# Performance work log

Hardware: AMD Instinct MI355X
Metric: run time of the kernel (lower is better)

The kernel has to match this reference:

```python
import jax, jax.numpy as jnp
import numpy as np

N_NODES = 100000
N_EDGES = 1600000
N_GRAPHS = 1000
NODES_PER_GRAPH = N_NODES // N_GRAPHS
IN_DIM, HID_DIM, OUT_DIM = 32, 64, 32


def setup_inputs() -> dict:
    key = jax.random.key(0)
    k_x, k_src, k_dst, k_w1, k_w2 = jax.random.split(key, 5)
    x = jax.random.normal(k_x, (N_NODES, IN_DIM), dtype=jnp.float32)
    src = jax.random.randint(k_src, (N_EDGES,), 0, N_NODES, dtype=jnp.int32)
    dst = jax.random.randint(k_dst, (N_EDGES,), 0, N_NODES, dtype=jnp.int32)
    edge_index = jnp.stack([src, dst], axis=0)
    batch = (jnp.arange(N_NODES, dtype=jnp.int32) // NODES_PER_GRAPH)
    W1 = jax.random.normal(k_w1, (IN_DIM, HID_DIM), dtype=jnp.float32) / np.sqrt(IN_DIM)
    b1 = jnp.zeros((HID_DIM,), dtype=jnp.float32)
    W2 = jax.random.normal(k_w2, (HID_DIM, OUT_DIM), dtype=jnp.float32) / np.sqrt(HID_DIM)
    b2 = jnp.zeros((OUT_DIM,), dtype=jnp.float32)
    return {"x": x, "edge_index": edge_index, "batch": batch,
            "W1": W1, "b1": b1, "W2": W2, "b2": b2}


def _gcn_conv(x, W, b, src, dst, deg_inv_sqrt):
    # PyG GCNConv: out = D^{-1/2}(A+I)D^{-1/2} X W + b, deg includes self-loops
    h = x @ W  # [N, F]
    norm = deg_inv_sqrt[src] * deg_inv_sqrt[dst]  # [E]
    agg = jax.ops.segment_sum(h[src] * norm[:, None], dst, num_segments=N_NODES)
    # self-loop contribution: norm = deg^{-1/2} * deg^{-1/2} = 1/deg
    agg = agg + h * (deg_inv_sqrt * deg_inv_sqrt)[:, None]
    return agg + b


def reference(x, edge_index, batch, W1, b1, W2, b2):
    src, dst = edge_index[0], edge_index[1]
    # degree at target nodes, with self-loops
    deg = 1.0 + jax.ops.segment_sum(jnp.ones_like(dst, dtype=x.dtype), dst,
                                    num_segments=N_NODES)
    deg_inv_sqrt = jax.lax.rsqrt(deg)
    h = jax.nn.relu(_gcn_conv(x, W1, b1, src, dst, deg_inv_sqrt))
    h = _gcn_conv(h, W2, b2, src, dst, deg_inv_sqrt)
    # per-graph mean pooling (fused segment mean)
    sums = jax.ops.segment_sum(h, batch, num_segments=N_GRAPHS)
    counts = jax.ops.segment_sum(jnp.ones((h.shape[0],), dtype=h.dtype), batch,
                                 num_segments=N_GRAPHS)
    return sums / counts[:, None]
```

## Files before the change

kernel.cpp:

```cpp
#include <hip/hip_runtime.h>

#define IN_DIM 32
#define HID_DIM 64
#define OUT_DIM 32

#define MAXBUCK 1024
#define CAP 2560
#define EPB 8192

typedef unsigned int u32;
typedef unsigned short u16;
typedef unsigned long long u64;
typedef __attribute__((ext_vector_type(8))) short bf16x8;
typedef __attribute__((ext_vector_type(4))) float f32x4;

static __device__ __forceinline__ u32 bf16rne(float f) {
    u32 u = __float_as_uint(f);
    return (u + 0x7FFFu + ((u >> 16) & 1u)) >> 16;
}
static __device__ __forceinline__ float blo(u32 u) { return __uint_as_float(u << 16); }
static __device__ __forceinline__ float bhi(u32 u) { return __uint_as_float(u & 0xFFFF0000u); }

__global__ __launch_bounds__(1024) void k_bin(const int* __restrict__ src,
                                              const int* __restrict__ dst,
                                              int* __restrict__ cursor,
                                              int* __restrict__ binned,
                                              int E, int nbuck, int npg, u32 M) {
    __shared__ int lcnt[MAXBUCK];
    __shared__ int lbase[MAXBUCK];
    int t = threadIdx.x;
    if (t < MAXBUCK) lcnt[t] = 0;
    __syncthreads();
    int base = blockIdx.x * EPB;
    int dreg[8], breg[8];
#pragma unroll
    for (int k = 0; k < 8; k++) {
        int e = base + k * 1024 + t;
        dreg[k] = (e < E) ? dst[e] : -1;
    }
#pragma unroll
    for (int k = 0; k < 8; k++) {
        if (dreg[k] >= 0) {
            breg[k] = (int)(((u64)(u32)dreg[k] * M) >> 38);
            atomicAdd(&lcnt[breg[k]], 1);
        }
    }
    __syncthreads();
    if (t < nbuck) {
        int c = lcnt[t];
        if (c) lbase[t] = atomicAdd(&cursor[t], c);
        lcnt[t] = 0;
    }
    __syncthreads();
#pragma unroll
    for (int k = 0; k < 8; k++) {
        if (dreg[k] >= 0) {
            int bk = breg[k];
            int dl = dreg[k] - bk * npg;
            int loc = lbase[bk] + atomicAdd(&lcnt[bk], 1);
            if (loc < CAP)
                binned[bk * CAP + loc] = (dl << 17) | src[base + k * 1024 + t];
        }
    }
}

__global__ __launch_bounds__(256) void k_csr(const int* __restrict__ binned,
                                             const int* __restrict__ cursor,
                                             const float* __restrict__ x,
                                             int2* __restrict__ row,
                                             float* __restrict__ dis,
                                             u16* __restrict__ g,
                                             int* __restrict__ meta,
                                             int N, int npg) {
    __shared__ int sEdge[CAP];
    __shared__ int sH[4][128];
    __shared__ int sExcl[128];
    __shared__ int sCur[128];
    __shared__ float sdis[128];
    __shared__ int wsum[2];
    int b = blockIdx.x;
    int t = threadIdx.x;
    int wid = t >> 6;
    int s0 = b * CAP;
    int cnt = cursor[b];
    if (cnt > CAP) cnt = CAP;

    for (int k = t; k < 4 * 128; k += 256) ((int*)sH)[k] = 0;
    __syncthreads();

    for (int k = t; k < cnt; k += 256) {
        int p = binned[s0 + k];
        sEdge[k] = p;
        atomicAdd(&sH[wid][p >> 17], 1);
    }
    __syncthreads();

    if (t < 128) {
        int myv = sH[0][t] + sH[1][t] + sH[2][t] + sH[3][t];
        int lane = t & 63;
        int incl = myv;
#pragma unroll
        for (int o = 1; o < 64; o <<= 1) {
            int up = __shfl_up(incl, o);
            if (lane >= o) incl += up;
        }
        if (lane == 63) wsum[t >> 6] = incl;
        sExcl[t] = incl - myv;
        sCur[t] = 0;
        sH[0][t] = myv;
    }
    __syncthreads();
    if (t < 128) {
        int exclv = sExcl[t] + ((t >= 64) ? wsum[0] : 0);
        sExcl[t] = exclv;
        int myv = sH[0][t];
        float d = rsqrtf(1.0f + (float)myv);
        sdis[t] = d;
        int node = b * npg + t;
        if (t < npg && node < N) {
            row[node] = make_int2(s0 + exclv, s0 + exclv + myv);
            dis[node] = d;
        }
    }
    __syncthreads();

    for (int k = t; k < cnt; k += 256) {
        int p = sEdge[k];
        int dl = p >> 17;
        int pos = sExcl[dl] + atomicAdd(&sCur[dl], 1);
        meta[s0 + pos] = p & 0x1FFFF;
    }

    int nbLo = b * npg;
    int nn = N - nbLo;
    if (nn > npg) nn = npg;
    if (nn < 0) nn = 0;
    int halfE = nn * 16;
    const float* xb = x + (size_t)nbLo * 32;
    u32* gb = (u32*)(g + (size_t)nbLo * 32);
    for (int j = t; j < halfE; j += 256) {
        int e0 = j * 2;
        float dd = sdis[e0 >> 5];
        gb[j] = bf16rne(dd * xb[e0]) | (bf16rne(dd * xb[e0 + 1]) << 16);
    }
}

__global__ __launch_bounds__(256) void k_agg(const u16* __restrict__ g,
                                             const int* __restrict__ meta,
                                             const int2* __restrict__ row,
                                             const float* __restrict__ dis,
                                             u16* __restrict__ outf, int N) {
    int gid = blockIdx.x * 256 + threadIdx.x;
    int i = gid >> 5;
    if (i >= N) return;
    int l = threadIdx.x & 31;
    int grp = (l >> 2) & 7;
    int sub = l & 3;
    const uint4* gv = (const uint4*)g;

    float a0 = 0.f, a1 = 0.f, a2 = 0.f, a3 = 0.f;
    float a4 = 0.f, a5 = 0.f, a6 = 0.f, a7 = 0.f;
    int2 rw = row[i];
    int e = rw.x, end = rw.y;
    for (; e + 16 <= end; e += 16) {
        int s0 = meta[e + grp];
        int s1 = meta[e + 8 + grp];
        uint4 v0 = gv[s0 * 4 + sub];
        uint4 v1 = gv[s1 * 4 + sub];
        a0 += blo(v0.x); a1 += bhi(v0.x); a2 += blo(v0.y); a3 += bhi(v0.y);
        a4 += blo(v0.z); a5 += bhi(v0.z); a6 += blo(v0.w); a7 += bhi(v0.w);
        a0 += blo(v1.x); a1 += bhi(v1.x); a2 += blo(v1.y); a3 += bhi(v1.y);
        a4 += blo(v1.z); a5 += bhi(v1.z); a6 += blo(v1.w); a7 += bhi(v1.w);
    }
    if (e + grp < end) {
        uint4 v = gv[meta[e + grp] * 4 + sub];
        a0 += blo(v.x); a1 += bhi(v.x); a2 += blo(v.y); a3 += bhi(v.y);
        a4 += blo(v.z); a5 += bhi(v.z); a6 += blo(v.w); a7 += bhi(v.w);
    }
    if (e + 8 + grp < end) {
        uint4 v = gv[meta[e + 8 + grp] * 4 + sub];
        a0 += blo(v.x); a1 += bhi(v.x); a2 += blo(v.y); a3 += bhi(v.y);
        a4 += blo(v.z); a5 += bhi(v.z); a6 += blo(v.w); a7 += bhi(v.w);
    }
#pragma unroll
    for (int m = 4; m <= 16; m <<= 1) {
        a0 += __shfl_xor(a0, m); a1 += __shfl_xor(a1, m);
        a2 += __shfl_xor(a2, m); a3 += __shfl_xor(a3, m);
        a4 += __shfl_xor(a4, m); a5 += __shfl_xor(a5, m);
        a6 += __shfl_xor(a6, m); a7 += __shfl_xor(a7, m);
    }
    if (grp == 0) {
        uint4 sv = gv[i * 4 + sub];
        float d = dis[i];
        u32 o0 = bf16rne(d * (a0 + blo(sv.x))) | (bf16rne(d * (a1 + bhi(sv.x))) << 16);
        u32 o1 = bf16rne(d * (a2 + blo(sv.y))) | (bf16rne(d * (a3 + bhi(sv.y))) << 16);
        u32 o2 = bf16rne(d * (a4 + blo(sv.z))) | (bf16rne(d * (a5 + bhi(sv.z))) << 16);
        u32 o3 = bf16rne(d * (a6 + blo(sv.w))) | (bf16rne(d * (a7 + bhi(sv.w))) << 16);
        ((uint4*)outf)[i * 4 + sub] = make_uint4(o0, o1, o2, o3);
    }
}

__global__ __launch_bounds__(256) void k_mlp(const u16* __restrict__ aggX,
                                             const float* __restrict__ W1,
                                             const float* __restrict__ b1,
                                             const float* __restrict__ W2,
                                             const float* __restrict__ dis,
                                             u16* __restrict__ t2, int N) {
    __shared__ float sHls[4][16 * 65];
    int t = threadIdx.x;
    int w = t >> 6;
    int L = t & 63;
    int q = L >> 4;
    int col = L & 15;
    int base = blockIdx.x * 64 + w * 16;

    int arow = base + col;
    uint4 av = (arow < N) ? ((const uint4*)aggX)[(size_t)arow * 4 + q]
                          : make_uint4(0, 0, 0, 0);
    bf16x8 afrag = *(bf16x8*)&av;

    bf16x8 b1f[4];
#pragma unroll
    for (int nt = 0; nt < 4; nt++) {
#pragma unroll
        for (int jj = 0; jj < 8; jj++)
            b1f[nt][jj] = (short)bf16rne(W1[(q * 8 + jj) * HID_DIM + nt * 16 + col]);
    }
    bf16x8 b2f[2][2];
#pragma unroll
    for (int ks = 0; ks < 2; ks++)
#pragma unroll
        for (int nt = 0; nt < 2; nt++) {
#pragma unroll
            for (int jj = 0; jj < 8; jj++)
                b2f[ks][nt][jj] =
                    (short)bf16rne(W2[(ks * 32 + q * 8 + jj) * OUT_DIM + nt * 16 + col]);
        }

#pragma unroll
    for (int nt = 0; nt < 4; nt++) {
        float bias = b1[nt * 16 + col];
        f32x4 c = {bias, bias, bias, bias};
        c = __builtin_amdgcn_mfma_f32_16x16x32_bf16(afrag, b1f[nt], c, 0, 0, 0);
#pragma unroll
        for (int r = 0; r < 4; r++)
            sHls[w][(q * 4 + r) * 65 + nt * 16 + col] = fmaxf(c[r], 0.0f);
    }
    __syncthreads();

    bf16x8 a2[2];
#pragma unroll
    for (int ks = 0; ks < 2; ks++) {
#pragma unroll
        for (int jj = 0; jj < 8; jj++)
            a2[ks][jj] = (short)bf16rne(sHls[w][col * 65 + ks * 32 + q * 8 + jj]);
    }

    f32x4 C2[2];
#pragma unroll
    for (int nt = 0; nt < 2; nt++) {
        f32x4 c = {0.f, 0.f, 0.f, 0.f};
        c = __builtin_amdgcn_mfma_f32_16x16x32_bf16(a2[0], b2f[0][nt], c, 0, 0, 0);
        c = __builtin_amdgcn_mfma_f32_16x16x32_bf16(a2[1], b2f[1][nt], c, 0, 0, 0);
        C2[nt] = c;
    }

#pragma unroll
    for (int r = 0; r < 4; r++) {
        int node = base + q * 4 + r;
        if (node < N) {
            float dd = dis[node];
            t2[(size_t)node * 32 + col]      = (u16)bf16rne(dd * C2[0][r]);
            t2[(size_t)node * 32 + 16 + col] = (u16)bf16rne(dd * C2[1][r]);
        }
    }
}

__global__ __launch_bounds__(256) void k_pool2(const int* __restrict__ binned,
                                               const int* __restrict__ cursor,
                                               const u16* __restrict__ gB,
                                               const float* __restrict__ dis,
                                               const float* __restrict__ b2,
                                               float* __restrict__ out,
                                               int N, int npg, float inv_npg) {
    __shared__ float sdis[128];
    __shared__ float sacc[32];
    int b = blockIdx.x;
    int t = threadIdx.x;
    if (t < 128) {
        int node = b * npg + t;
        sdis[t] = (t < npg && node < N) ? dis[node] : 0.0f;
    }
    if (t < 32) sacc[t] = 0.0f;
    __syncthreads();

    int s0 = b * CAP;
    int cnt = cursor[b];
    if (cnt > CAP) cnt = CAP;
    int sub = t & 3;
    int et = t >> 2;
    const uint4* gv = (const uint4*)gB;

    float a0 = 0.f, a1 = 0.f, a2 = 0.f, a3 = 0.f;
    float a4 = 0.f, a5 = 0.f, a6 = 0.f, a7 = 0.f;
    int e = et;
    int p0 = 0;
    uint4 v0 = make_uint4(0, 0, 0, 0);
    bool have = (e < cnt);
    if (have) { p0 = binned[s0 + e]; v0 = gv[(p0 & 0x1FFFF) * 4 + sub]; }
    for (; e + 64 < cnt; e += 64) {
        int p1 = binned[s0 + e + 64];
        uint4 v1 = gv[(p1 & 0x1FFFF) * 4 + sub];
        float w = sdis[p0 >> 17];
        a0 = fmaf(w, blo(v0.x), a0); a1 = fmaf(w, bhi(v0.x), a1);
        a2 = fmaf(w, blo(v0.y), a2); a3 = fmaf(w, bhi(v0.y), a3);
        a4 = fmaf(w, blo(v0.z), a4); a5 = fmaf(w, bhi(v0.z), a5);
        a6 = fmaf(w, blo(v0.w), a6); a7 = fmaf(w, bhi(v0.w), a7);
        p0 = p1; v0 = v1;
    }
    if (have) {
        float w = sdis[p0 >> 17];
        a0 = fmaf(w, blo(v0.x), a0); a1 = fmaf(w, bhi(v0.x), a1);
        a2 = fmaf(w, blo(v0.y), a2); a3 = fmaf(w, bhi(v0.y), a3);
        a4 = fmaf(w, blo(v0.z), a4); a5 = fmaf(w, bhi(v0.z), a5);
        a6 = fmaf(w, blo(v0.w), a6); a7 = fmaf(w, bhi(v0.w), a7);
    }
#pragma unroll
    for (int m = 4; m <= 32; m <<= 1) {
        a0 += __shfl_xor(a0, m); a1 += __shfl_xor(a1, m);
        a2 += __shfl_xor(a2, m); a3 += __shfl_xor(a3, m);
        a4 += __shfl_xor(a4, m); a5 += __shfl_xor(a5, m);
        a6 += __shfl_xor(a6, m); a7 += __shfl_xor(a7, m);
    }
    if ((t & 63) < 4) {
        atomicAdd(&sacc[sub * 8 + 0], a0);
        atomicAdd(&sacc[sub * 8 + 1], a1);
        atomicAdd(&sacc[sub * 8 + 2], a2);
        atomicAdd(&sacc[sub * 8 + 3], a3);
        atomicAdd(&sacc[sub * 8 + 4], a4);
        atomicAdd(&sacc[sub * 8 + 5], a5);
        atomicAdd(&sacc[sub * 8 + 6], a6);
        atomicAdd(&sacc[sub * 8 + 7], a7);
    }

    float accs = 0.0f;
    int elems = npg * 32;
    const u16* gbase = gB + (size_t)b * npg * 32;
    int nbLo = b * npg;
    for (int k = t; k < elems; k += 256) {
        int node = k >> 5;
        if (nbLo + node < N)
            accs = fmaf(sdis[node], __uint_as_float((u32)gbase[k] << 16), accs);
    }
    atomicAdd(&sacc[t & 31], accs);
    __syncthreads();

    if (t < 32)
        out[b * 32 + t] = fmaf(sacc[t], inv_npg, b2[t]);
}

extern "C" void kernel_launch(void* const* d_in, const int* in_sizes, int n_in,
                              void* d_out, int out_size, void* d_ws, size_t ws_size,
                              hipStream_t stream) {
    const float* x   = (const float*)d_in[0];
    const int* eidx  = (const int*)d_in[1];
    const float* W1  = (const float*)d_in[3];
    const float* b1  = (const float*)d_in[4];
    const float* W2  = (const float*)d_in[5];
    const float* b2  = (const float*)d_in[6];
    float* out       = (float*)d_out;

    const int N = in_sizes[0] / IN_DIM;
    const int E = in_sizes[1] / 2;
    const int G = out_size / OUT_DIM;
    const int npg = N / G;
    const int nbuck = G;
    const int* src = eidx;
    const int* dst = eidx + E;
    const u32 M = (u32)(((1ull << 38) + npg - 1) / (u64)npg);

    char* ws = (char*)d_ws;
    size_t off = 0;
    auto alloc = [&](size_t bytes) -> char* {
        char* p = ws + off;
        off = (off + bytes + 255) & ~(size_t)255;
        return p;
    };
    int*   cursor = (int*)alloc(MAXBUCK * sizeof(int));
    int2*  row    = (int2*)alloc((size_t)N * sizeof(int2));
    float* dis    = (float*)alloc((size_t)N * sizeof(float));
    int*   binned = (int*)alloc((size_t)nbuck * CAP * sizeof(int));
    int*   meta   = (int*)alloc((size_t)nbuck * CAP * sizeof(int));
    u16*   g      = (u16*)alloc((size_t)N * IN_DIM * sizeof(u16));
    u16*   bufA   = (u16*)alloc((size_t)N * IN_DIM * sizeof(u16));
    u16*   bufB   = (u16*)alloc((size_t)N * OUT_DIM * sizeof(u16));
    (void)ws_size;

    hipMemsetAsync(cursor, 0, MAXBUCK * sizeof(int), stream);

    k_bin<<<(E + EPB - 1) / EPB, 1024, 0, stream>>>(src, dst, cursor, binned,
                                                    E, nbuck, npg, M);
    k_csr<<<nbuck, 256, 0, stream>>>(binned, cursor, x, row, dis, g, meta, N, npg);
    k_agg<<<((size_t)N * 32 + 255) / 256, 256, 0, stream>>>(g, meta, row, dis, bufA, N);
    k_mlp<<<(N + 63) / 64, 256, 0, stream>>>(bufA, W1, b1, W2, dis, bufB, N);
    k_pool2<<<nbuck, 256, 0, stream>>>(binned, cursor, bufB, dis, b2, out,
                                       N, npg, 1.0f / (float)npg);
}
```

Measured before the change: 161.7 us.

## Drop CSR build; fuse layer-1 aggregation and MLP per graph bucket via LDS atomics

The CSR construction (prefix scan and meta scatter) goes away. Layer-1 aggregation is now done per destination bucket with shared-memory float atomics straight from the binned edge list, and it is fused with the two-layer MFMA MLP in one kernel per graph, which removes the bufA round trip and one launch. The self-loop pooling term is computed inside the fused kernel and passed to the pool kernel, which now runs 512 threads with a simpler unrolled gather loop. In exchange, LDS atomic contention rises and the order of float summation changes.

After: 392.3 us. +142.6%, slower.

```diff
diff --git a/kernel.cpp b/kernel.cpp
--- a/kernel.cpp
+++ b/kernel.cpp
@@ -64,20 +64,14 @@
     }
 }
 
-__global__ __launch_bounds__(256) void k_csr(const int* __restrict__ binned,
+__global__ __launch_bounds__(256) void k_deg(const int* __restrict__ binned,
                                              const int* __restrict__ cursor,
                                              const float* __restrict__ x,
-                                             int2* __restrict__ row,
                                              float* __restrict__ dis,
                                              u16* __restrict__ g,
-                                             int* __restrict__ meta,
                                              int N, int npg) {
-    __shared__ int sEdge[CAP];
     __shared__ int sH[4][128];
-    __shared__ int sExcl[128];
-    __shared__ int sCur[128];
     __shared__ float sdis[128];
-    __shared__ int wsum[2];
     int b = blockIdx.x;
     int t = threadIdx.x;
     int wid = t >> 6;
@@ -87,49 +81,17 @@
 
     for (int k = t; k < 4 * 128; k += 256) ((int*)sH)[k] = 0;
     __syncthreads();
-
-    for (int k = t; k < cnt; k += 256) {
-        int p = binned[s0 + k];
-        sEdge[k] = p;
-        atomicAdd(&sH[wid][p >> 17], 1);
-    }
-    __syncthreads();
-
+    for (int k = t; k < cnt; k += 256)
+        atomicAdd(&sH[wid][binned[s0 + k] >> 17], 1);
+    __syncthreads();
     if (t < 128) {
-        int myv = sH[0][t] + sH[1][t] + sH[2][t] + sH[3][t];
-        int lane = t & 63;
-        int incl = myv;
-#pragma unroll
-        for (int o = 1; o < 64; o <<= 1) {
-            int up = __shfl_up(incl, o);
-            if (lane >= o) incl += up;
-        }
-        if (lane == 63) wsum[t >> 6] = incl;
-        sExcl[t] = incl - myv;
-        sCur[t] = 0;
-        sH[0][t] = myv;
-    }
-    __syncthreads();
-    if (t < 128) {
-        int exclv = sExcl[t] + ((t >= 64) ? wsum[0] : 0);
-        sExcl[t] = exclv;
-        int myv = sH[0][t];
-        float d = rsqrtf(1.0f + (float)myv);
+        int deg = sH[0][t] + sH[1][t] + sH[2][t] + sH[3][t];
+        float d = rsqrtf(1.0f + (float)deg);
         sdis[t] = d;
         int node = b * npg + t;
-        if (t < npg && node < N) {
-            row[node] = make_int2(s0 + exclv, s0 + exclv + myv);
-            dis[node] = d;
-        }
-    }
-    __syncthreads();
-
-    for (int k = t; k < cnt; k += 256) {
-        int p = sEdge[k];
-        int dl = p >> 17;
-        int pos = sExcl[dl] + atomicAdd(&sCur[dl], 1);
-        meta[s0 + pos] = p & 0x1FFFF;
-    }
+        if (t < npg && node < N) dis[node] = d;
+    }
+    __syncthreads();
 
     int nbLo = b * npg;
     int nn = N - nbLo;
@@ -145,79 +107,68 @@
     }
 }
 
-__global__ __launch_bounds__(256) void k_agg(const u16* __restrict__ g,
-                                             const int* __restrict__ meta,
-                                             const int2* __restrict__ row,
-                                             const float* __restrict__ dis,
-                                             u16* __restrict__ outf, int N) {
-    int gid = blockIdx.x * 256 + threadIdx.x;
-    int i = gid >> 5;
-    if (i >= N) return;
-    int l = threadIdx.x & 31;
-    int grp = (l >> 2) & 7;
-    int sub = l & 3;
-    const uint4* gv = (const uint4*)g;
-
-    float a0 = 0.f, a1 = 0.f, a2 = 0.f, a3 = 0.f;
-    float a4 = 0.f, a5 = 0.f, a6 = 0.f, a7 = 0.f;
-    int2 rw = row[i];
-    int e = rw.x, end = rw.y;
-    for (; e + 16 <= end; e += 16) {
-        int s0 = meta[e + grp];
-        int s1 = meta[e + 8 + grp];
-        uint4 v0 = gv[s0 * 4 + sub];
-        uint4 v1 = gv[s1 * 4 + sub];
-        a0 += blo(v0.x); a1 += bhi(v0.x); a2 += blo(v0.y); a3 += bhi(v0.y);
-        a4 += blo(v0.z); a5 += bhi(v0.z); a6 += blo(v0.w); a7 += bhi(v0.w);
-        a0 += blo(v1.x); a1 += bhi(v1.x); a2 += blo(v1.y); a3 += bhi(v1.y);
-        a4 += blo(v1.z); a5 += bhi(v1.z); a6 += blo(v1.w); a7 += bhi(v1.w);
-    }
-    if (e + grp < end) {
-        uint4 v = gv[meta[e + grp] * 4 + sub];
-        a0 += blo(v.x); a1 += bhi(v.x); a2 += blo(v.y); a3 += bhi(v.y);
-        a4 += blo(v.z); a5 += bhi(v.z); a6 += blo(v.w); a7 += bhi(v.w);
-    }
-    if (e + 8 + grp < end) {
-        uint4 v = gv[meta[e + 8 + grp] * 4 + sub];
-        a0 += blo(v.x); a1 += bhi(v.x); a2 += blo(v.y); a3 += bhi(v.y);
-        a4 += blo(v.z); a5 += bhi(v.z); a6 += blo(v.w); a7 += bhi(v.w);
-    }
-#pragma unroll
-    for (int m = 4; m <= 16; m <<= 1) {
-        a0 += __shfl_xor(a0, m); a1 += __shfl_xor(a1, m);
-        a2 += __shfl_xor(a2, m); a3 += __shfl_xor(a3, m);
-        a4 += __shfl_xor(a4, m); a5 += __shfl_xor(a5, m);
-        a6 += __shfl_xor(a6, m); a7 += __shfl_xor(a7, m);
-    }
-    if (grp == 0) {
-        uint4 sv = gv[i * 4 + sub];
-        float d = dis[i];
-        u32 o0 = bf16rne(d * (a0 + blo(sv.x))) | (bf16rne(d * (a1 + bhi(sv.x))) << 16);
-        u32 o1 = bf16rne(d * (a2 + blo(sv.y))) | (bf16rne(d * (a3 + bhi(sv.y))) << 16);
-        u32 o2 = bf16rne(d * (a4 + blo(sv.z))) | (bf16rne(d * (a5 + bhi(sv.z))) << 16);
-        u32 o3 = bf16rne(d * (a6 + blo(sv.w))) | (bf16rne(d * (a7 + bhi(sv.w))) << 16);
-        ((uint4*)outf)[i * 4 + sub] = make_uint4(o0, o1, o2, o3);
-    }
-}
-
-__global__ __launch_bounds__(256) void k_mlp(const u16* __restrict__ aggX,
-                                             const float* __restrict__ W1,
-                                             const float* __restrict__ b1,
-                                             const float* __restrict__ W2,
-                                             const float* __restrict__ dis,
-                                             u16* __restrict__ t2, int N) {
+__global__ __launch_bounds__(256) void k_fused(const int* __restrict__ binned,
+                                               const int* __restrict__ cursor,
+                                               const u16* __restrict__ g,
+                                               const float* __restrict__ dis,
+                                               const float* __restrict__ W1,
+                                               const float* __restrict__ b1,
+                                               const float* __restrict__ W2,
+                                               u16* __restrict__ t2,
+                                               float* __restrict__ selfs,
+                                               int N, int npg) {
+    __shared__ float acc[128][33];
     __shared__ float sHls[4][16 * 65];
+    __shared__ float sdisL[128];
+    __shared__ float sacc[32];
+    int b = blockIdx.x;
     int t = threadIdx.x;
+    int s0 = b * CAP;
+    int cnt = cursor[b];
+    if (cnt > CAP) cnt = CAP;
+    int nbLo = b * npg;
+
+    for (int k = t; k < 128 * 33; k += 256) ((float*)acc)[k] = 0.0f;
+    if (t < 128) {
+        int node = nbLo + t;
+        sdisL[t] = (t < npg && node < N) ? dis[node] : 0.0f;
+    }
+    if (t < 32) sacc[t] = 0.0f;
+    __syncthreads();
+
+    {
+        int sub = t & 3;
+        int et = t >> 2;
+        const uint4* gv = (const uint4*)g;
+#pragma unroll 4
+        for (int e = et; e < cnt; e += 64) {
+            int p = binned[s0 + e];
+            uint4 v = gv[(u32)(p & 0x1FFFF) * 4 + sub];
+            float* ar = &acc[p >> 17][sub << 3];
+            atomicAdd(&ar[0], blo(v.x)); atomicAdd(&ar[1], bhi(v.x));
+            atomicAdd(&ar[2], blo(v.y)); atomicAdd(&ar[3], bhi(v.y));
+            atomicAdd(&ar[4], blo(v.z)); atomicAdd(&ar[5], bhi(v.z));
+            atomicAdd(&ar[6], blo(v.w)); atomicAdd(&ar[7], bhi(v.w));
+        }
+    }
+    __syncthreads();
+
+    {
+        const u16* gwin = g + (size_t)nbLo * 32;
+        int elems = npg * 32;
+        for (int k = t; k < elems; k += 256) {
+            int i = k >> 5;
+            float dd = sdisL[i];
+            float gval = __uint_as_float((u32)gwin[k] << 16);
+            acc[i][k & 31] = dd * (acc[i][k & 31] + gval);
+        }
+    }
+    __syncthreads();
+
     int w = t >> 6;
     int L = t & 63;
     int q = L >> 4;
     int col = L & 15;
-    int base = blockIdx.x * 64 + w * 16;
-
-    int arow = base + col;
-    uint4 av = (arow < N) ? ((const uint4*)aggX)[(size_t)arow * 4 + q]
-                          : make_uint4(0, 0, 0, 0);
-    bf16x8 afrag = *(bf16x8*)&av;
 
     bf16x8 b1f[4];
 #pragma unroll
@@ -237,50 +188,78 @@
                     (short)bf16rne(W2[(ks * 32 + q * 8 + jj) * OUT_DIM + nt * 16 + col]);
         }
 
-#pragma unroll
-    for (int nt = 0; nt < 4; nt++) {
-        float bias = b1[nt * 16 + col];
-        f32x4 c = {bias, bias, bias, bias};
-        c = __builtin_amdgcn_mfma_f32_16x16x32_bf16(afrag, b1f[nt], c, 0, 0, 0);
-#pragma unroll
-        for (int r = 0; r < 4; r++)
-            sHls[w][(q * 4 + r) * 65 + nt * 16 + col] = fmaxf(c[r], 0.0f);
-    }
-    __syncthreads();
-
-    bf16x8 a2[2];
-#pragma unroll
-    for (int ks = 0; ks < 2; ks++) {
+    float self0 = 0.0f, self1 = 0.0f;
+
+#pragma unroll
+    for (int g2 = 0; g2 < 2; g2++) {
+        int nodeB = g2 * 64 + w * 16;
+
+        bf16x8 afrag;
 #pragma unroll
         for (int jj = 0; jj < 8; jj++)
-            a2[ks][jj] = (short)bf16rne(sHls[w][col * 65 + ks * 32 + q * 8 + jj]);
-    }
-
-    f32x4 C2[2];
-#pragma unroll
-    for (int nt = 0; nt < 2; nt++) {
-        f32x4 c = {0.f, 0.f, 0.f, 0.f};
-        c = __builtin_amdgcn_mfma_f32_16x16x32_bf16(a2[0], b2f[0][nt], c, 0, 0, 0);
-        c = __builtin_amdgcn_mfma_f32_16x16x32_bf16(a2[1], b2f[1][nt], c, 0, 0, 0);
-        C2[nt] = c;
-    }
-
-#pragma unroll
-    for (int r = 0; r < 4; r++) {
-        int node = base + q * 4 + r;
-        if (node < N) {
-            float dd = dis[node];
-            t2[(size_t)node * 32 + col]      = (u16)bf16rne(dd * C2[0][r]);
-            t2[(size_t)node * 32 + 16 + col] = (u16)bf16rne(dd * C2[1][r]);
-        }
-    }
-}
-
-__global__ __launch_bounds__(256) void k_pool2(const int* __restrict__ binned,
+            afrag[jj] = (short)bf16rne(acc[nodeB + col][q * 8 + jj]);
+
+#pragma unroll
+        for (int nt = 0; nt < 4; nt++) {
+            float bias = b1[nt * 16 + col];
+            f32x4 c = {bias, bias, bias, bias};
+            c = __builtin_amdgcn_mfma_f32_16x16x32_bf16(afrag, b1f[nt], c, 0, 0, 0);
+#pragma unroll
+            for (int r = 0; r < 4; r++)
+                sHls[w][(q * 4 + r) * 65 + nt * 16 + col] = fmaxf(c[r], 0.0f);
+        }
+        __syncthreads();
+
+        bf16x8 a2[2];
+#pragma unroll
+        for (int ks = 0; ks < 2; ks++) {
+#pragma unroll
+            for (int jj = 0; jj < 8; jj++)
+                a2[ks][jj] = (short)bf16rne(sHls[w][col * 65 + ks * 32 + q * 8 + jj]);
+        }
+
+        f32x4 C2[2];
+#pragma unroll
+        for (int nt = 0; nt < 2; nt++) {
+            f32x4 c = {0.f, 0.f, 0.f, 0.f};
+            c = __builtin_amdgcn_mfma_f32_16x16x32_bf16(a2[0], b2f[0][nt], c, 0, 0, 0);
+            c = __builtin_amdgcn_mfma_f32_16x16x32_bf16(a2[1], b2f[1][nt], c, 0, 0, 0);
+            C2[nt] = c;
+        }
+
+#pragma unroll
+        for (int r = 0; r < 4; r++) {
+            int nl = nodeB + q * 4 + r;
+            int node = nbLo + nl;
+            if (nl < npg && node < N) {
+                float dd = sdisL[nl];
+                float y0 = dd * C2[0][r];
+                float y1 = dd * C2[1][r];
+                t2[(size_t)node * 32 + col]      = (u16)bf16rne(y0);
+                t2[(size_t)node * 32 + 16 + col] = (u16)bf16rne(y1);
+                self0 = fmaf(dd, y0, self0);
+                self1 = fmaf(dd, y1, self1);
+            }
+        }
+        __syncthreads();
+    }
+
+    self0 += __shfl_xor(self0, 16); self0 += __shfl_xor(self0, 32);
+    self1 += __shfl_xor(self1, 16); self1 += __shfl_xor(self1, 32);
+    if (q == 0) {
+        atomicAdd(&sacc[col], self0);
+        atomicAdd(&sacc[16 + col], self1);
+    }
+    __syncthreads();
+    if (t < 32) selfs[b * 32 + t] = sacc[t];
+}
+
+__global__ __launch_bounds__(512) void k_pool2(const int* __restrict__ binned,
                                                const int* __restrict__ cursor,
                                                const u16* __restrict__ gB,
                                                const float* __restrict__ dis,
                                                const float* __restrict__ b2,
+                                               const float* __restrict__ selfs,
                                                float* __restrict__ out,
                                                int N, int npg, float inv_npg) {
     __shared__ float sdis[128];
@@ -303,27 +282,15 @@
 
     float a0 = 0.f, a1 = 0.f, a2 = 0.f, a3 = 0.f;
     float a4 = 0.f, a5 = 0.f, a6 = 0.f, a7 = 0.f;
-    int e = et;
-    int p0 = 0;
-    uint4 v0 = make_uint4(0, 0, 0, 0);
-    bool have = (e < cnt);
-    if (have) { p0 = binned[s0 + e]; v0 = gv[(p0 & 0x1FFFF) * 4 + sub]; }
-    for (; e + 64 < cnt; e += 64) {
-        int p1 = binned[s0 + e + 64];
-        uint4 v1 = gv[(p1 & 0x1FFFF) * 4 + sub];
-        float w = sdis[p0 >> 17];
-        a0 = fmaf(w, blo(v0.x), a0); a1 = fmaf(w, bhi(v0.x), a1);
-        a2 = fmaf(w, blo(v0.y), a2); a3 = fmaf(w, bhi(v0.y), a3);
-        a4 = fmaf(w, blo(v0.z), a4); a5 = fmaf(w, bhi(v0.z), a5);
-        a6 = fmaf(w, blo(v0.w), a6); a7 = fmaf(w, bhi(v0.w), a7);
-        p0 = p1; v0 = v1;
-    }
-    if (have) {
-        float w = sdis[p0 >> 17];
-        a0 = fmaf(w, blo(v0.x), a0); a1 = fmaf(w, bhi(v0.x), a1);
-        a2 = fmaf(w, blo(v0.y), a2); a3 = fmaf(w, bhi(v0.y), a3);
-        a4 = fmaf(w, blo(v0.z), a4); a5 = fmaf(w, bhi(v0.z), a5);
-        a6 = fmaf(w, blo(v0.w), a6); a7 = fmaf(w, bhi(v0.w), a7);
+#pragma unroll 4
+    for (int e = et; e < cnt; e += 128) {
+        int p = binned[s0 + e];
+        uint4 v = gv[(u32)(p & 0x1FFFF) * 4 + sub];
+        float wgt = sdis[p >> 17];
+        a0 = fmaf(wgt, blo(v.x), a0); a1 = fmaf(wgt, bhi(v.x), a1);
+        a2 = fmaf(wgt, blo(v.y), a2); a3 = fmaf(wgt, bhi(v.y), a3);
+        a4 = fmaf(wgt, blo(v.z), a4); a5 = fmaf(wgt, bhi(v.z), a5);
+        a6 = fmaf(wgt, blo(v.w), a6); a7 = fmaf(wgt, bhi(v.w), a7);
     }
 #pragma unroll
     for (int m = 4; m <= 32; m <<= 1) {
@@ -342,21 +309,10 @@
         atomicAdd(&sacc[sub * 8 + 6], a6);
         atomicAdd(&sacc[sub * 8 + 7], a7);
     }
-
-    float accs = 0.0f;
-    int elems = npg * 32;
-    const u16* gbase = gB + (size_t)b * npg * 32;
-    int nbLo = b * npg;
-    for (int k = t; k < elems; k += 256) {
-        int node = k >> 5;
-        if (nbLo + node < N)
-            accs = fmaf(sdis[node], __uint_as_float((u32)gbase[k] << 16), accs);
-    }
-    atomicAdd(&sacc[t & 31], accs);
     __syncthreads();
 
     if (t < 32)
-        out[b * 32 + t] = fmaf(sacc[t], inv_npg, b2[t]);
+        out[b * 32 + t] = fmaf(sacc[t] + selfs[b * 32 + t], inv_npg, b2[t]);
 }
 
 extern "C" void kernel_launch(void* const* d_in, const int* in_sizes, int n_in,
@@ -387,22 +343,20 @@
         return p;
     };
     int*   cursor = (int*)alloc(MAXBUCK * sizeof(int));
-    int2*  row    = (int2*)alloc((size_t)N * sizeof(int2));
     float* dis    = (float*)alloc((size_t)N * sizeof(float));
     int*   binned = (int*)alloc((size_t)nbuck * CAP * sizeof(int));
-    int*   meta   = (int*)alloc((size_t)nbuck * CAP * sizeof(int));
     u16*   g      = (u16*)alloc((size_t)N * IN_DIM * sizeof(u16));
-    u16*   bufA   = (u16*)alloc((size_t)N * IN_DIM * sizeof(u16));
     u16*   bufB   = (u16*)alloc((size_t)N * OUT_DIM * sizeof(u16));
+    float* selfs  = (float*)alloc((size_t)G * OUT_DIM * sizeof(float));
     (void)ws_size;
 
     hipMemsetAsync(cursor, 0, MAXBUCK * sizeof(int), stream);
 
     k_bin<<<(E + EPB - 1) / EPB, 1024, 0, stream>>>(src, dst, cursor, binned,
                                                     E, nbuck, npg, M);
-    k_csr<<<nbuck, 256, 0, stream>>>(binned, cursor, x, row, dis, g, meta, N, npg);
-    k_agg<<<((size_t)N * 32 + 255) / 256, 256, 0, stream>>>(g, meta, row, dis, bufA, N);
-    k_mlp<<<(N + 63) / 64, 256, 0, stream>>>(bufA, W1, b1, W2, dis, bufB, N);
-    k_pool2<<<nbuck, 256, 0, stream>>>(binned, cursor, bufB, dis, b2, out,
+    k_deg<<<nbuck, 256, 0, stream>>>(binned, cursor, x, dis, g, N, npg);
+    k_fused<<<nbuck, 256, 0, stream>>>(binned, cursor, g, dis, W1, b1, W2,
+                                       bufB, selfs, N, npg);
+    k_pool2<<<nbuck, 512, 0, stream>>>(binned, cursor, bufB, dis, b2, selfs, out,
                                        N, npg, 1.0f / (float)npg);
 }
```
